# Performance work log

Hardware: AMD Instinct MI355X
Metric: run time of the kernel (lower is better)

Reference implementation:

```python
import jax, jax.numpy as jnp
import numpy as np

N = 50000

def gcn_conv(x, W, b, src, dst, n_nodes):
    # PyG GCNConv: h = x @ W; add self-loops; sym-normalize; scatter-add; + bias
    h = x @ W  # [N, d_out]
    loop = jnp.arange(n_nodes, dtype=src.dtype)
    s = jnp.concatenate([src, loop])
    d = jnp.concatenate([dst, loop])
    deg = jax.ops.segment_sum(jnp.ones_like(d, dtype=h.dtype), d, num_segments=n_nodes)
    dinv = jnp.where(deg > 0, jax.lax.rsqrt(deg), 0.0)
    norm = dinv[s] * dinv[d]  # [E+N]
    msgs = h[s] * norm[:, None]  # gather + scale
    out = jax.ops.segment_sum(msgs, d, num_segments=n_nodes)  # scatter-add
    return out + b

def setup_inputs() -> dict:
    key = jax.random.key(0)
    k1, k2, k3, k4 = jax.random.split(key, 4)
    in_c, hid_c, out_c, E = 512, 256, 64, 800000
    x = jax.random.normal(k1, (N, in_c), dtype=jnp.float32)
    edge_index = jax.random.randint(k2, (2, E), 0, N, dtype=jnp.int64)
    W1 = jax.random.normal(k3, (in_c, hid_c), dtype=jnp.float32) / np.sqrt(in_c)
    b1 = jnp.zeros((hid_c,), dtype=jnp.float32)
    W2 = jax.random.normal(k4, (hid_c, out_c), dtype=jnp.float32) / np.sqrt(hid_c)
    b2 = jnp.zeros((out_c,), dtype=jnp.float32)
    return {"x": x, "edge_index": edge_index, "W1": W1, "b1": b1, "W2": W2, "b2": b2}

def reference(x, edge_index, W1, b1, W2, b2):
    src, dst = edge_index[0], edge_index[1]
    h = gcn_conv(x, W1, b1, src, dst, N)
    h = jax.nn.relu(h)
    h = gcn_conv(h, W2, b2, src, dst, N)
    return jax.nn.log_softmax(h, axis=1)
```

## Files before the change

kernel.cpp:

```cpp
#include <hip/hip_runtime.h>
#include <hip/hip_bf16.h>

#define IN_C 512
#define HID_C 256
#define OUT_C 64

typedef __attribute__((ext_vector_type(8))) short bf16x8;
typedef __attribute__((ext_vector_type(4))) float f32x4;
typedef __attribute__((ext_vector_type(2))) float f32x2;

__device__ __forceinline__ ushort f2bf(float f) {
  __hip_bfloat16 h = __float2bfloat16(f);
  union { __hip_bfloat16 h; ushort u; } v; v.h = h; return v.u;
}
__device__ __forceinline__ float u2f(uint u) {
  union { uint i; float f; } v; v.i = u; return v.f;
}
__device__ __forceinline__ void pkacc(f32x2& aLo, f32x2& aHi, uint ux, uint uy) {
  f32x2 lo, hi;
  lo[0] = u2f(ux << 16);         lo[1] = u2f(uy << 16);
  hi[0] = u2f(ux & 0xffff0000u); hi[1] = u2f(uy & 0xffff0000u);
  aLo += lo;
  aHi += hi;
}
__device__ __forceinline__ void glds16(const ushort* g, ushort* l) {
  __builtin_amdgcn_global_load_lds(
      (const __attribute__((address_space(1))) unsigned int*)(const void*)g,
      (__attribute__((address_space(3))) unsigned int*)(void*)l, 16, 0, 0);
}


__global__ void deg_count(const int* __restrict__ dst, int* __restrict__ counts, int E) {
  int e = blockIdx.x * 256 + threadIdx.x;
  if (e >= E) return;
  atomicAdd(&counts[dst[e]], 1);
}

#define SCAN_TILE 1024

__global__ __launch_bounds__(256) void scan_block_sums(const int* __restrict__ counts,
                                                       int* __restrict__ partial, int n) {
  int base = blockIdx.x * SCAN_TILE + threadIdx.x * 4;
  int s = 0;
  if (base + 3 < n) {
    int4 v = *(const int4*)(counts + base);
    s = v.x + v.y + v.z + v.w;
  } else {
#pragma unroll
    for (int i = 0; i < 4; ++i) if (base + i < n) s += counts[base + i];
  }
#pragma unroll
  for (int off = 1; off < 64; off <<= 1) s += __shfl_xor(s, off);
  __shared__ int ws[4];
  int lane = threadIdx.x & 63, wid = threadIdx.x >> 6;
  if (lane == 0) ws[wid] = s;
  __syncthreads();
  if (threadIdx.x == 0) partial[blockIdx.x] = ws[0] + ws[1] + ws[2] + ws[3];
}

__global__ void scan_partials(int* __restrict__ partial, int nb) {
  int lane = threadIdx.x;
  int carry = 0;
  for (int base = 0; base < nb; base += 64) {
    int i = base + lane;
    int v = (i < nb) ? partial[i] : 0;
    int incl = v;
#pragma unroll
    for (int off = 1; off < 64; off <<= 1) {
      int y = __shfl_up(incl, off);
      if (lane >= off) incl += y;
    }
    if (i < nb) partial[i] = carry + incl - v;
    carry += __shfl(incl, 63);
  }
}

__global__ __launch_bounds__(256) void scan_write(const int* __restrict__ counts,
                                                  const int* __restrict__ partial,
                                                  int* __restrict__ offs,
                                                  int* __restrict__ cur,
                                                  float* __restrict__ dinv,
                                                  int n, int E) {
  int tid = threadIdx.x;
  int base = blockIdx.x * SCAN_TILE + tid * 4;
  int4 c = make_int4(0, 0, 0, 0);
  if (base + 3 < n) {
    c = *(const int4*)(counts + base);
  } else {
    if (base + 0 < n) c.x = counts[base + 0];
    if (base + 1 < n) c.y = counts[base + 1];
    if (base + 2 < n) c.z = counts[base + 2];
  }
  int tsum = c.x + c.y + c.z + c.w;
  int lane = tid & 63, wid = tid >> 6;
  int incl = tsum;
#pragma unroll
  for (int off = 1; off < 64; off <<= 1) {
    int y = __shfl_up(incl, off);
    if (lane >= off) incl += y;
  }
  __shared__ int ws[4];
  if (lane == 63) ws[wid] = incl;
  __syncthreads();
  int wbase = 0;
#pragma unroll
  for (int w = 0; w < 4; ++w) if (w < wid) wbase += ws[w];
  int off0 = partial[blockIdx.x] + wbase + (incl - tsum);
  int4 ov;
  ov.x = off0;
  ov.y = off0 + c.x;
  ov.z = off0 + c.x + c.y;
  ov.w = off0 + c.x + c.y + c.z;
  float4 dv;
  dv.x = rsqrtf((float)(c.x + 1));
  dv.y = rsqrtf((float)(c.y + 1));
  dv.z = rsqrtf((float)(c.z + 1));
  dv.w = rsqrtf((float)(c.w + 1));
  if (base + 3 < n) {
    *(int4*)(offs + base) = ov;
    *(int4*)(cur + base) = ov;
    *(float4*)(dinv + base) = dv;
  } else {
    int o4[4] = {ov.x, ov.y, ov.z, ov.w};
    float d4[4] = {dv.x, dv.y, dv.z, dv.w};
    for (int i = 0; i < 4; ++i)
      if (base + i < n) { offs[base + i] = o4[i]; cur[base + i] = o4[i]; dinv[base + i] = d4[i]; }
  }
  if (blockIdx.x == 0 && tid == 0) offs[n] = E;
}

__global__ void fill_adj(const int* __restrict__ src, const int* __restrict__ dst,
                         int* __restrict__ cur, int* __restrict__ adj, int E) {
  int e = blockIdx.x * 256 + threadIdx.x;
  if (e >= E) return;
  int pos = atomicAdd(&cur[dst[e]], 1);
  adj[pos] = src[e];
}

__global__ void convert_wt(const float* __restrict__ W, ushort* __restrict__ Wt, int K, int Ncol) {
  int idx = blockIdx.x * 256 + threadIdx.x;
  if (idx >= K * Ncol) return;
  int n = idx / K, k = idx % K;
  Wt[idx] = f2bf(W[(size_t)k * Ncol + n]);
}

__global__ __launch_bounds__(256) void convert_x(const float* __restrict__ x,
                                                 ushort* __restrict__ xb, long n8) {
  long stride = (long)gridDim.x * 256;
  for (long i = (long)blockIdx.x * 256 + threadIdx.x; i < n8; i += stride) {
    const float4* p = (const float4*)(x + i * 8);
    float4 v0 = p[0], v1 = p[1];
    uint4 o;
    o.x = (uint)f2bf(v0.x) | ((uint)f2bf(v0.y) << 16);
    o.y = (uint)f2bf(v0.z) | ((uint)f2bf(v0.w) << 16);
    o.z = (uint)f2bf(v1.x) | ((uint)f2bf(v1.y) << 16);
    o.w = (uint)f2bf(v1.z) | ((uint)f2bf(v1.w) << 16);
    *(uint4*)(xb + i * 8) = o;
  }
}


__global__ __launch_bounds__(256) void gemm1_bf(const ushort* __restrict__ A,
                                                const ushort* __restrict__ Bt,
                                                const float* __restrict__ dinv,
                                                ushort* __restrict__ C, int M) {
  __shared__ __align__(16) ushort As[2][128 * 32];
  __shared__ __align__(16) ushort Bs[2][128 * 32];
  int tid = threadIdx.x;
  int lane = tid & 63, wid = tid >> 6;
  int m0 = blockIdx.x * 128;
  int n0 = blockIdx.y * 128;
  int ca = wid * 64 + lane;
  int rowa0 = ca >> 2, cola0 = (ca & 3) * 8;
  int rowa1 = (ca + 256) >> 2, cola1 = (ca & 3) * 8;
  int gma0 = m0 + rowa0; if (gma0 >= M) gma0 = M - 1;
  int gma1 = m0 + rowa1; if (gma1 >= M) gma1 = M - 1;
  const ushort* gA0 = A + (size_t)gma0 * IN_C + cola0;
  const ushort* gA1 = A + (size_t)gma1 * IN_C + cola1;
  const ushort* gB0 = Bt + (size_t)(n0 + rowa0) * IN_C + cola0;
  const ushort* gB1 = Bt + (size_t)(n0 + rowa1) * IN_C + cola1;

  int wm = (wid >> 1) * 64, wn = (wid & 1) * 64;
  int kf = (lane >> 4) * 8, rl = lane & 15;
  f32x4 acc[4][4] = {};

  glds16(gA0, &As[0][ca * 8]);
  glds16(gA1, &As[0][ca * 8 + 2048]);
  glds16(gB0, &Bs[0][ca * 8]);
  glds16(gB1, &Bs[0][ca * 8 + 2048]);
  __syncthreads();

  int cur = 0;
  for (int t = 0; t < 16; ++t) {
    if (t < 15) {
      int k0 = (t + 1) * 32;
      int nxt = cur ^ 1;
      glds16(gA0 + k0, &As[nxt][ca * 8]);
      glds16(gA1 + k0, &As[nxt][ca * 8 + 2048]);
      glds16(gB0 + k0, &Bs[nxt][ca * 8]);
      glds16(gB1 + k0, &Bs[nxt][ca * 8 + 2048]);
    }
    bf16x8 a[4], b[4];
#pragma unroll
    for (int i = 0; i < 4; ++i)
      a[i] = *(const bf16x8*)&As[cur][(wm + i * 16 + rl) * 32 + kf];
#pragma unroll
    for (int j = 0; j < 4; ++j)
      b[j] = *(const bf16x8*)&Bs[cur][(wn + j * 16 + rl) * 32 + kf];
#pragma unroll
    for (int i = 0; i < 4; ++i)
#pragma unroll
      for (int j = 0; j < 4; ++j)
        acc[i][j] = __builtin_amdgcn_mfma_f32_16x16x32_bf16(a[i], b[j], acc[i][j], 0, 0, 0);
    __syncthreads();
    cur ^= 1;
  }

  int r4 = (lane >> 4) * 4;
  int cl = lane & 15;
#pragma unroll
  for (int i = 0; i < 4; ++i) {
#pragma unroll
    for (int r = 0; r < 4; ++r) {
      int gr = m0 + wm + i * 16 + r4 + r;
      if (gr < M) {
        float dv = dinv[gr];
#pragma unroll
        for (int j = 0; j < 4; ++j) {
          int gc = n0 + wn + j * 16 + cl;
          C[(size_t)gr * HID_C + gc] = f2bf(dv * acc[i][j][r]);
        }
      }
    }
  }
}

__global__ __launch_bounds__(256) void gemm2(const ushort* __restrict__ A,
                                             const ushort* __restrict__ Bt,
                                             const float* __restrict__ dinv,
                                             ushort* __restrict__ C, int M) {
  __shared__ __align__(16) ushort As[2][128 * 32];
  __shared__ __align__(16) ushort Bs[2][64 * 32];
  int tid = threadIdx.x;
  int lane = tid & 63, wid = tid >> 6;
  int m0 = blockIdx.x * 128;
  int ca = wid * 64 + lane;
  int rowa0 = ca >> 2, cola0 = (ca & 3) * 8;
  int rowa1 = (ca + 256) >> 2;
  int gma0 = m0 + rowa0; if (gma0 >= M) gma0 = M - 1;
  int gma1 = m0 + rowa1; if (gma1 >= M) gma1 = M - 1;
  const ushort* gA0 = A + (size_t)gma0 * HID_C + cola0;
  const ushort* gA1 = A + (size_t)gma1 * HID_C + cola0;
  const ushort* gB0 = Bt + (size_t)rowa0 * HID_C + cola0;

  int wm = wid * 32;
  int kf = (lane >> 4) * 8, rl = lane & 15;
  f32x4 acc[2][4] = {};

  glds16(gA0, &As[0][ca * 8]);
  glds16(gA1, &As[0][ca * 8 + 2048]);
  glds16(gB0, &Bs[0][ca * 8]);
  __syncthreads();

  int cur = 0;
  for (int t = 0; t < 8; ++t) {
    if (t < 7) {
      int k0 = (t + 1) * 32;
      int nxt = cur ^ 1;
      glds16(gA0 + k0, &As[nxt][ca * 8]);
      glds16(gA1 + k0, &As[nxt][ca * 8 + 2048]);
      glds16(gB0 + k0, &Bs[nxt][ca * 8]);
    }
    bf16x8 a[2], b[4];
#pragma unroll
    for (int i = 0; i < 2; ++i)
      a[i] = *(const bf16x8*)&As[cur][(wm + i * 16 + rl) * 32 + kf];
#pragma unroll
    for (int j = 0; j < 4; ++j)
      b[j] = *(const bf16x8*)&Bs[cur][(j * 16 + rl) * 32 + kf];
#pragma unroll
    for (int i = 0; i < 2; ++i)
#pragma unroll
      for (int j = 0; j < 4; ++j)
        acc[i][j] = __builtin_amdgcn_mfma_f32_16x16x32_bf16(a[i], b[j], acc[i][j], 0, 0, 0);
    __syncthreads();
    cur ^= 1;
  }

  int r4 = (lane >> 4) * 4;
  int cl = lane & 15;
#pragma unroll
  for (int i = 0; i < 2; ++i) {
#pragma unroll
    for (int r = 0; r < 4; ++r) {
      int gr = m0 + wm + i * 16 + r4 + r;
      if (gr < M) {
        float dv = dinv[gr];
#pragma unroll
        for (int j = 0; j < 4; ++j) {
          int gc = j * 16 + cl;
          C[(size_t)gr * OUT_C + gc] = f2bf(dv * acc[i][j][r]);
        }
      }
    }
  }
}


__global__ __launch_bounds__(256) void agg1(const ushort* __restrict__ h,
                                            ushort* __restrict__ out,
                                            const float* __restrict__ dinv,
                                            const int* __restrict__ offs,
                                            const int* __restrict__ adj,
                                            const float* __restrict__ bias, int Nn) {
  int node = blockIdx.x * 4 + (threadIdx.x >> 6);
  if (node >= Nn) return;
  int lane = threadIdx.x & 63;
  int slot = lane >> 4;
  int c0 = (lane & 15) * 16;
  int e0 = offs[node];
  int cnt = offs[node + 1] - e0 + 1;
  const ushort* hc = h + c0;
  f32x2 aLo[4] = {}, aHi[4] = {};
  for (int b0 = 0; b0 < cnt; b0 += 64) {
    int vk = b0 + lane;
    int myadj = node;
    if (vk > 0 && vk < cnt) myadj = adj[e0 + vk - 1];
    int bn = cnt - b0; if (bn > 64) bn = 64;
    int iters = (bn + 3) >> 2;
#pragma unroll 2
    for (int i = 0; i < iters; ++i) {
      int k = slot + 4 * i;
      int s = __shfl(myadj, k < bn ? k : 0);
      if (k < bn) {
        const uint4* rp = (const uint4*)(hc + (size_t)s * HID_C);
        uint4 u0 = rp[0];
        uint4 u1 = rp[1];
        pkacc(aLo[0], aHi[0], u0.x, u0.y);
        pkacc(aLo[1], aHi[1], u0.z, u0.w);
        pkacc(aLo[2], aHi[2], u1.x, u1.y);
        pkacc(aLo[3], aHi[3], u1.z, u1.w);
      }
    }
  }
  float r16[16];
#pragma unroll
  for (int q = 0; q < 4; ++q) {
    r16[4 * q + 0] = aLo[q][0];
    r16[4 * q + 1] = aHi[q][0];
    r16[4 * q + 2] = aLo[q][1];
    r16[4 * q + 3] = aHi[q][1];
  }
#pragma unroll
  for (int i = 0; i < 16; ++i) {
    r16[i] += __shfl_xor(r16[i], 16);
    r16[i] += __shfl_xor(r16[i], 32);
  }
  if (lane < 16) {
    float dv = dinv[node];
    const float4* bp = (const float4*)(bias + c0);
    float bb[16];
#pragma unroll
    for (int q = 0; q < 4; ++q) {
      float4 b4 = bp[q];
      bb[q * 4 + 0] = b4.x; bb[q * 4 + 1] = b4.y;
      bb[q * 4 + 2] = b4.z; bb[q * 4 + 3] = b4.w;
    }
    uint r[8];
#pragma unroll
    for (int i = 0; i < 8; ++i) {
      float v0 = fmaxf(dv * r16[2 * i]     + bb[2 * i],     0.f);
      float v1 = fmaxf(dv * r16[2 * i + 1] + bb[2 * i + 1], 0.f);
      r[i] = (uint)f2bf(v0) | ((uint)f2bf(v1) << 16);
    }
    uint4* op = (uint4*)(out + (size_t)node * HID_C + c0);
    op[0] = make_uint4(r[0], r[1], r[2], r[3]);
    op[1] = make_uint4(r[4], r[5], r[6], r[7]);
  }
}

__global__ __launch_bounds__(256) void agg2(const ushort* __restrict__ h,
                                            float* __restrict__ out,
                                            const float* __restrict__ dinv,
                                            const int* __restrict__ offs,
                                            const int* __restrict__ adj,
                                            const float* __restrict__ bias, int Nn) {
  int node = blockIdx.x * 4 + (threadIdx.x >> 6);
  if (node >= Nn) return;
  int lane = threadIdx.x & 63;
  int slot = lane >> 3;
  int c0 = (lane & 7) * 8;
  int e0 = offs[node];
  int cnt = offs[node + 1] - e0 + 1;
  const ushort* hc = h + c0;
  f32x2 aLo[2] = {}, aHi[2] = {};
  for (int b0 = 0; b0 < cnt; b0 += 64) {
    int vk = b0 + lane;
    int myadj = node;
    if (vk > 0 && vk < cnt) myadj = adj[e0 + vk - 1];
    int bn = cnt - b0; if (bn > 64) bn = 64;
    int iters = (bn + 7) >> 3;
#pragma unroll 2
    for (int i = 0; i < iters; ++i) {
      int k = slot + 8 * i;
      int s = __shfl(myadj, k < bn ? k : 0);
      if (k < bn) {
        uint4 u = *(const uint4*)(hc + (size_t)s * OUT_C);
        pkacc(aLo[0], aHi[0], u.x, u.y);
        pkacc(aLo[1], aHi[1], u.z, u.w);
      }
    }
  }
  float r8[8];
#pragma unroll
  for (int q = 0; q < 2; ++q) {
    r8[4 * q + 0] = aLo[q][0];
    r8[4 * q + 1] = aHi[q][0];
    r8[4 * q + 2] = aLo[q][1];
    r8[4 * q + 3] = aHi[q][1];
  }
#pragma unroll
  for (int i = 0; i < 8; ++i) {
    r8[i] += __shfl_xor(r8[i], 8);
    r8[i] += __shfl_xor(r8[i], 16);
    r8[i] += __shfl_xor(r8[i], 32);
  }
  float dv = dinv[node];
  const float4* bp = (const float4*)(bias + c0);
  float4 bb0 = bp[0], bb1 = bp[1];
  float v[8];
  v[0] = dv * r8[0] + bb0.x; v[1] = dv * r8[1] + bb0.y;
  v[2] = dv * r8[2] + bb0.z; v[3] = dv * r8[3] + bb0.w;
  v[4] = dv * r8[4] + bb1.x; v[5] = dv * r8[5] + bb1.y;
  v[6] = dv * r8[6] + bb1.z; v[7] = dv * r8[7] + bb1.w;
  float m = v[0];
#pragma unroll
  for (int i = 1; i < 8; ++i) m = fmaxf(m, v[i]);
  m = fmaxf(m, __shfl_xor(m, 1));
  m = fmaxf(m, __shfl_xor(m, 2));
  m = fmaxf(m, __shfl_xor(m, 4));
  float s8 = 0.f;
#pragma unroll
  for (int i = 0; i < 8; ++i) s8 += expf(v[i] - m);
  s8 += __shfl_xor(s8, 1);
  s8 += __shfl_xor(s8, 2);
  s8 += __shfl_xor(s8, 4);
  float lg = logf(s8);
  if (lane < 8) {
    float4* op = (float4*)(out + (size_t)node * OUT_C + c0);
    op[0] = make_float4(v[0] - m - lg, v[1] - m - lg, v[2] - m - lg, v[3] - m - lg);
    op[1] = make_float4(v[4] - m - lg, v[5] - m - lg, v[6] - m - lg, v[7] - m - lg);
  }
}


extern "C" void kernel_launch(void* const* d_in, const int* in_sizes, int n_in,
                              void* d_out, int out_size, void* d_ws, size_t ws_size,
                              hipStream_t stream) {
  const float* x  = (const float*)d_in[0];
  const int*   ei = (const int*)d_in[1];
  const float* W1 = (const float*)d_in[2];
  const float* b1 = (const float*)d_in[3];
  const float* W2 = (const float*)d_in[4];
  const float* b2 = (const float*)d_in[5];
  float* outp = (float*)d_out;

  int Nn = in_sizes[0] / IN_C;
  int E  = in_sizes[1] / 2;
  const int* srcv = ei;
  const int* dstv = ei + E;

  char* ws = (char*)d_ws;
  size_t o = 0;
  auto alloc = [&](size_t bytes) {
    char* p = ws + o;
    o = (o + bytes + 255) & ~(size_t)255;
    return p;
  };
  float*  dinv  = (float*)alloc((size_t)Nn * 4);
  int*    counts= (int*)alloc((size_t)Nn * 4);
  int*    offs  = (int*)alloc((size_t)(Nn + 1) * 4);
  int*    cur   = (int*)alloc((size_t)Nn * 4);
  int*    adj   = (int*)alloc((size_t)E * 4);
  int*    partial=(int*)alloc((size_t)((Nn + SCAN_TILE - 1) / SCAN_TILE) * 4);
  ushort* W1t   = (ushort*)alloc((size_t)IN_C * HID_C * 2);
  ushort* W2t   = (ushort*)alloc((size_t)HID_C * OUT_C * 2);
  ushort* h1p   = (ushort*)alloc((size_t)Nn * HID_C * 2);
  ushort* h1a   = (ushort*)alloc((size_t)Nn * HID_C * 2);
  ushort* h2p   = (ushort*)alloc((size_t)Nn * OUT_C * 2);
  size_t xb_bytes = (size_t)Nn * IN_C * 2;
  bool use_bf = (o + xb_bytes) <= ws_size;
  ushort* xb = use_bf ? (ushort*)alloc(xb_bytes) : nullptr;

  int eb = (E + 255) / 256;
  int sb = (Nn + SCAN_TILE - 1) / SCAN_TILE;

  hipMemsetAsync(counts, 0, (size_t)Nn * 4, stream);
  deg_count<<<eb, 256, 0, stream>>>(dstv, counts, E);
  scan_block_sums<<<sb, 256, 0, stream>>>(counts, partial, Nn);
  scan_partials<<<1, 64, 0, stream>>>(partial, sb);
  scan_write<<<sb, 256, 0, stream>>>(counts, partial, offs, cur, dinv, Nn, E);
  fill_adj<<<eb, 256, 0, stream>>>(srcv, dstv, cur, adj, E);
  convert_wt<<<(IN_C * HID_C + 255) / 256, 256, 0, stream>>>(W1, W1t, IN_C, HID_C);
  convert_wt<<<(HID_C * OUT_C + 255) / 256, 256, 0, stream>>>(W2, W2t, HID_C, OUT_C);

  if (use_bf) {
    long n8 = (long)Nn * IN_C / 8;
    int cb = (int)((n8 + 255) / 256); if (cb > 2048) cb = 2048;
    convert_x<<<cb, 256, 0, stream>>>(x, xb, n8);
    gemm1_bf<<<dim3((Nn + 127) / 128, HID_C / 128), 256, 0, stream>>>(xb, W1t, dinv, h1p, Nn);
  } else {
    gemm1_bf<<<dim3((Nn + 127) / 128, HID_C / 128), 256, 0, stream>>>((const ushort*)x, W1t, dinv, h1p, Nn);
  }
  agg1<<<(Nn + 3) / 4, 256, 0, stream>>>(h1p, h1a, dinv, offs, adj, b1, Nn);
  gemm2<<<(Nn + 127) / 128, 256, 0, stream>>>(h1a, W2t, dinv, h2p, Nn);
  agg2<<<(Nn + 3) / 4, 256, 0, stream>>>(h2p, outp, dinv, offs, adj, b2, Nn);
}
```

Baseline: 255.6 us.

## Fuse fp32-to-bf16 conversion of x into a full-width GEMM1 tile

Drops the separate convert_x pass. GEMM1 now loads fp32 x directly through registers, packs it to bf16 and stores it into LDS after the MFMAs, which overlaps the conversion with compute. Each block covers the full 256-column output with 512 threads, so x is read once instead of once per column tile, and the bf16 copy of x is no longer written to and re-read from memory. The weight transpose now goes through a coalesced LDS tile, and the aggregation loops unroll by 4. The cost is register-path A loads in place of direct-to-LDS loads, plus higher LDS use and a larger block that may lower occupancy.

```diff
diff --git a/kernel.cpp b/kernel.cpp
--- a/kernel.cpp
+++ b/kernel.cpp
@@ -12,6 +12,9 @@
 __device__ __forceinline__ ushort f2bf(float f) {
   __hip_bfloat16 h = __float2bfloat16(f);
   union { __hip_bfloat16 h; ushort u; } v; v.h = h; return v.u;
+}
+__device__ __forceinline__ uint pack2bf(float a, float b) {
+  return (uint)f2bf(a) | ((uint)f2bf(b) << 16);
 }
 __device__ __forceinline__ float u2f(uint u) {
   union { uint i; float f; } v; v.i = u; return v.f;
@@ -137,81 +140,88 @@
   adj[pos] = src[e];
 }
 
-__global__ void convert_wt(const float* __restrict__ W, ushort* __restrict__ Wt, int K, int Ncol) {
-  int idx = blockIdx.x * 256 + threadIdx.x;
-  if (idx >= K * Ncol) return;
-  int n = idx / K, k = idx % K;
-  Wt[idx] = f2bf(W[(size_t)k * Ncol + n]);
-}
-
-__global__ __launch_bounds__(256) void convert_x(const float* __restrict__ x,
-                                                 ushort* __restrict__ xb, long n8) {
-  long stride = (long)gridDim.x * 256;
-  for (long i = (long)blockIdx.x * 256 + threadIdx.x; i < n8; i += stride) {
-    const float4* p = (const float4*)(x + i * 8);
-    float4 v0 = p[0], v1 = p[1];
-    uint4 o;
-    o.x = (uint)f2bf(v0.x) | ((uint)f2bf(v0.y) << 16);
-    o.y = (uint)f2bf(v0.z) | ((uint)f2bf(v0.w) << 16);
-    o.z = (uint)f2bf(v1.x) | ((uint)f2bf(v1.y) << 16);
-    o.w = (uint)f2bf(v1.z) | ((uint)f2bf(v1.w) << 16);
-    *(uint4*)(xb + i * 8) = o;
-  }
-}
-
-
-__global__ __launch_bounds__(256) void gemm1_bf(const ushort* __restrict__ A,
+__global__ __launch_bounds__(256) void transpose_w(const float* __restrict__ W,
+                                                   ushort* __restrict__ Wt, int K, int N) {
+  __shared__ ushort t[32][33];
+  int n0 = blockIdx.x * 32;
+  int k0 = blockIdx.y * 32;
+  int tx = threadIdx.x & 31;
+  int ty = threadIdx.x >> 5;
+#pragma unroll
+  for (int i = 0; i < 4; ++i) {
+    int k = k0 + ty + i * 8;
+    t[ty + i * 8][tx] = f2bf(W[(size_t)k * N + n0 + tx]);
+  }
+  __syncthreads();
+#pragma unroll
+  for (int i = 0; i < 4; ++i) {
+    int n = n0 + ty + i * 8;
+    Wt[(size_t)n * K + k0 + tx] = t[tx][ty + i * 8];
+  }
+}
+
+
+__global__ __launch_bounds__(512) void gemm1_fs(const float* __restrict__ A,
                                                 const ushort* __restrict__ Bt,
                                                 const float* __restrict__ dinv,
                                                 ushort* __restrict__ C, int M) {
   __shared__ __align__(16) ushort As[2][128 * 32];
-  __shared__ __align__(16) ushort Bs[2][128 * 32];
+  __shared__ __align__(16) ushort Bs[2][256 * 32];
   int tid = threadIdx.x;
   int lane = tid & 63, wid = tid >> 6;
   int m0 = blockIdx.x * 128;
-  int n0 = blockIdx.y * 128;
-  int ca = wid * 64 + lane;
-  int rowa0 = ca >> 2, cola0 = (ca & 3) * 8;
-  int rowa1 = (ca + 256) >> 2, cola1 = (ca & 3) * 8;
-  int gma0 = m0 + rowa0; if (gma0 >= M) gma0 = M - 1;
-  int gma1 = m0 + rowa1; if (gma1 >= M) gma1 = M - 1;
-  const ushort* gA0 = A + (size_t)gma0 * IN_C + cola0;
-  const ushort* gA1 = A + (size_t)gma1 * IN_C + cola1;
-  const ushort* gB0 = Bt + (size_t)(n0 + rowa0) * IN_C + cola0;
-  const ushort* gB1 = Bt + (size_t)(n0 + rowa1) * IN_C + cola1;
-
-  int wm = (wid >> 1) * 64, wn = (wid & 1) * 64;
+  int arow = tid >> 2, acol = (tid & 3) * 8;
+  int gma = m0 + arow; if (gma >= M) gma = M - 1;
+  const float* gA = A + (size_t)gma * IN_C + acol;
+  int rb0 = tid >> 2, cb0 = (tid & 3) * 8;
+  int rb1 = (tid + 512) >> 2;
+  const ushort* gB0 = Bt + (size_t)rb0 * IN_C + cb0;
+  const ushort* gB1 = Bt + (size_t)rb1 * IN_C + cb0;
+
+  int wr = wid >> 2, wc = wid & 3;
   int kf = (lane >> 4) * 8, rl = lane & 15;
   f32x4 acc[4][4] = {};
 
-  glds16(gA0, &As[0][ca * 8]);
-  glds16(gA1, &As[0][ca * 8 + 2048]);
-  glds16(gB0, &Bs[0][ca * 8]);
-  glds16(gB1, &Bs[0][ca * 8 + 2048]);
+  {
+    float4 p0 = *(const float4*)gA;
+    float4 p1 = *(const float4*)(gA + 4);
+    glds16(gB0, &Bs[0][tid * 8]);
+    glds16(gB1, &Bs[0][(tid + 512) * 8]);
+    uint4 w;
+    w.x = pack2bf(p0.x, p0.y); w.y = pack2bf(p0.z, p0.w);
+    w.z = pack2bf(p1.x, p1.y); w.w = pack2bf(p1.z, p1.w);
+    *(uint4*)&As[0][arow * 32 + acol] = w;
+  }
   __syncthreads();
 
   int cur = 0;
   for (int t = 0; t < 16; ++t) {
+    float4 p0, p1;
     if (t < 15) {
-      int k0 = (t + 1) * 32;
-      int nxt = cur ^ 1;
-      glds16(gA0 + k0, &As[nxt][ca * 8]);
-      glds16(gA1 + k0, &As[nxt][ca * 8 + 2048]);
-      glds16(gB0 + k0, &Bs[nxt][ca * 8]);
-      glds16(gB1 + k0, &Bs[nxt][ca * 8 + 2048]);
-    }
-    bf16x8 a[4], b[4];
+      const float* g = gA + (t + 1) * 32;
+      p0 = *(const float4*)g;
+      p1 = *(const float4*)(g + 4);
+      glds16(gB0 + (t + 1) * 32, &Bs[cur ^ 1][tid * 8]);
+      glds16(gB1 + (t + 1) * 32, &Bs[cur ^ 1][(tid + 512) * 8]);
+    }
+    bf16x8 af[4], bf[4];
 #pragma unroll
     for (int i = 0; i < 4; ++i)
-      a[i] = *(const bf16x8*)&As[cur][(wm + i * 16 + rl) * 32 + kf];
+      af[i] = *(const bf16x8*)&As[cur][(wr * 64 + i * 16 + rl) * 32 + kf];
 #pragma unroll
     for (int j = 0; j < 4; ++j)
-      b[j] = *(const bf16x8*)&Bs[cur][(wn + j * 16 + rl) * 32 + kf];
+      bf[j] = *(const bf16x8*)&Bs[cur][(wc * 64 + j * 16 + rl) * 32 + kf];
 #pragma unroll
     for (int i = 0; i < 4; ++i)
 #pragma unroll
       for (int j = 0; j < 4; ++j)
-        acc[i][j] = __builtin_amdgcn_mfma_f32_16x16x32_bf16(a[i], b[j], acc[i][j], 0, 0, 0);
+        acc[i][j] = __builtin_amdgcn_mfma_f32_16x16x32_bf16(af[i], bf[j], acc[i][j], 0, 0, 0);
+    if (t < 15) {
+      uint4 w;
+      w.x = pack2bf(p0.x, p0.y); w.y = pack2bf(p0.z, p0.w);
+      w.z = pack2bf(p1.x, p1.y); w.w = pack2bf(p1.z, p1.w);
+      *(uint4*)&As[cur ^ 1][arow * 32 + acol] = w;
+    }
     __syncthreads();
     cur ^= 1;
   }
@@ -222,12 +232,12 @@
   for (int i = 0; i < 4; ++i) {
 #pragma unroll
     for (int r = 0; r < 4; ++r) {
-      int gr = m0 + wm + i * 16 + r4 + r;
+      int gr = m0 + wr * 64 + i * 16 + r4 + r;
       if (gr < M) {
         float dv = dinv[gr];
 #pragma unroll
         for (int j = 0; j < 4; ++j) {
-          int gc = n0 + wn + j * 16 + cl;
+          int gc = wc * 64 + j * 16 + cl;
           C[(size_t)gr * HID_C + gc] = f2bf(dv * acc[i][j][r]);
         }
       }
@@ -328,7 +338,7 @@
     if (vk > 0 && vk < cnt) myadj = adj[e0 + vk - 1];
     int bn = cnt - b0; if (bn > 64) bn = 64;
     int iters = (bn + 3) >> 2;
-#pragma unroll 2
+#pragma unroll 4
     for (int i = 0; i < iters; ++i) {
       int k = slot + 4 * i;
       int s = __shfl(myadj, k < bn ? k : 0);
@@ -400,7 +410,7 @@
     if (vk > 0 && vk < cnt) myadj = adj[e0 + vk - 1];
     int bn = cnt - b0; if (bn > 64) bn = 64;
     int iters = (bn + 7) >> 3;
-#pragma unroll 2
+#pragma unroll 4
     for (int i = 0; i < iters; ++i) {
       int k = slot + 8 * i;
       int s = __shfl(myadj, k < bn ? k : 0);
@@ -488,9 +498,6 @@
   ushort* h1p   = (ushort*)alloc((size_t)Nn * HID_C * 2);
   ushort* h1a   = (ushort*)alloc((size_t)Nn * HID_C * 2);
   ushort* h2p   = (ushort*)alloc((size_t)Nn * OUT_C * 2);
-  size_t xb_bytes = (size_t)Nn * IN_C * 2;
-  bool use_bf = (o + xb_bytes) <= ws_size;
-  ushort* xb = use_bf ? (ushort*)alloc(xb_bytes) : nullptr;
 
   int eb = (E + 255) / 256;
   int sb = (Nn + SCAN_TILE - 1) / SCAN_TILE;
@@ -501,17 +508,10 @@
   scan_partials<<<1, 64, 0, stream>>>(partial, sb);
   scan_write<<<sb, 256, 0, stream>>>(counts, partial, offs, cur, dinv, Nn, E);
   fill_adj<<<eb, 256, 0, stream>>>(srcv, dstv, cur, adj, E);
-  convert_wt<<<(IN_C * HID_C + 255) / 256, 256, 0, stream>>>(W1, W1t, IN_C, HID_C);
-  convert_wt<<<(HID_C * OUT_C + 255) / 256, 256, 0, stream>>>(W2, W2t, HID_C, OUT_C);
-
-  if (use_bf) {
-    long n8 = (long)Nn * IN_C / 8;
-    int cb = (int)((n8 + 255) / 256); if (cb > 2048) cb = 2048;
-    convert_x<<<cb, 256, 0, stream>>>(x, xb, n8);
-    gemm1_bf<<<dim3((Nn + 127) / 128, HID_C / 128), 256, 0, stream>>>(xb, W1t, dinv, h1p, Nn);
-  } else {
-    gemm1_bf<<<dim3((Nn + 127) / 128, HID_C / 128), 256, 0, stream>>>((const ushort*)x, W1t, dinv, h1p, Nn);
-  }
+  transpose_w<<<dim3(HID_C / 32, IN_C / 32), 256, 0, stream>>>(W1, W1t, IN_C, HID_C);
+  transpose_w<<<dim3(OUT_C / 32, HID_C / 32), 256, 0, stream>>>(W2, W2t, HID_C, OUT_C);
+
+  gemm1_fs<<<(Nn + 127) / 128, 512, 0, stream>>>(x, W1t, dinv, h1p, Nn);
   agg1<<<(Nn + 3) / 4, 256, 0, stream>>>(h1p, h1a, dinv, offs, adj, b1, Nn);
   gemm2<<<(Nn + 127) / 128, 256, 0, stream>>>(h1a, W2t, dinv, h2p, Nn);
   agg2<<<(Nn + 3) / 4, 256, 0, stream>>>(h2p, outp, dinv, offs, adj, b2, Nn);
```

Result: faster. 231.7 us (-9.4%).
